# Kernel tuning notes

Hardware: AMD Instinct MI355X
Metric: run time of the kernel (lower is better)

## Reference

```python
import jax, jax.numpy as jnp
import numpy as np

N = 4096
M = 1024
APPERTURE = 250
L1, L2, L3, PRED = 1024, 512, 128, 1
EPS = 1e-6


def _layer_norm(x, gamma, beta):
    # torch x.std(-1) is unbiased (ddof=1)
    mean = jnp.mean(x, axis=-1, keepdims=True)
    std = jnp.std(x, axis=-1, ddof=1, keepdims=True)
    return gamma * (x - mean) / (std + EPS) + beta


def _self_attention(x, Wq, Wk, Wv, Wo, band_mask):
    # x: [n, m]; Linear(bias=False) => x @ W.T
    K = x @ Wk.T
    Q = (x @ Wq.T) * 0.06
    V = x @ Wv.T
    logits = Q @ K.T                      # [n, n]
    logits = jnp.where(band_mask, logits, -jnp.inf)  # keep |i-j| < apperture
    att = jax.nn.softmax(logits, axis=-1)
    # original: y = (V^T @ att)^T == att^T @ V  (note the transpose!)
    y = att.T @ V
    return y @ Wo.T, att


def setup_inputs() -> dict:
    key = jax.random.key(0)
    ks = jax.random.split(key, 20)
    s = 0.02
    inp = {
        'x1': jax.random.normal(ks[0], (1, N, M), jnp.float32),
        'x2': jax.random.normal(ks[1], (1, N, M), jnp.float32),
        'x3': jax.random.normal(ks[2], (1, N, M), jnp.float32),
        'Wq': jax.random.normal(ks[3], (M, M), jnp.float32) * s,
        'Wk': jax.random.normal(ks[4], (M, M), jnp.float32) * s,
        'Wv': jax.random.normal(ks[5], (M, M), jnp.float32) * s,
        'Wo': jax.random.normal(ks[6], (M, M), jnp.float32) * s,
        'ka_w': jax.random.normal(ks[7], (L1, M), jnp.float32) * s,
        'ka_b': jnp.zeros((L1,), jnp.float32),
        'kb_w': jax.random.normal(ks[8], (L2, L1), jnp.float32) * s,
        'kb_b': jnp.zeros((L2,), jnp.float32),
        'kc_w': jax.random.normal(ks[9], (L3, L2), jnp.float32) * s,
        'kc_b': jnp.zeros((L3,), jnp.float32),
        'kd_w': jax.random.normal(ks[10], (PRED, L3), jnp.float32) * s,
        'kd_b': jnp.zeros((PRED,), jnp.float32),
        'g13': jnp.ones((M,), jnp.float32),
        'b13': jnp.zeros((M,), jnp.float32),
        'gkc': jnp.ones((L3,), jnp.float32),
        'bkc': jnp.zeros((L3,), jnp.float32),
        'seq_len': N,
    }
    return inp


def reference(x1, x2, x3, Wq, Wk, Wv, Wo, ka_w, ka_b, kb_w, kb_b, kc_w, kc_b,
              kd_w, kd_b, g13, b13, gkc, bkc, seq_len):
    x1 = x1.reshape(-1, x1.shape[2])
    x2 = x2.reshape(-1, x2.shape[2])
    x3 = x3.reshape(-1, x3.shape[2])
    n = x1.shape[0]
    idx = jnp.arange(n)
    band_mask = jnp.abs(idx[:, None] - idx[None, :]) < APPERTURE  # allowed

    y1, att1 = _self_attention(x1, Wq, Wk, Wv, Wo, band_mask)
    y2, _ = _self_attention(x2, Wq, Wk, Wv, Wo, band_mask)
    y3, _ = _self_attention(x3, Wq, Wk, Wv, Wo, band_mask)

    # residual + (dropout == identity in eval) + shared LayerNorm
    y1 = _layer_norm(y1 + x1, g13, b13)
    y2 = _layer_norm(y2 + x2, g13, b13)
    y3 = _layer_norm(y3 + x3, g13, b13)

    y = y1 + y2 + y3  # cmb == [1,1,1]
    y = y @ ka_w.T + ka_b
    y = y @ kb_w.T + kb_b
    y = jax.nn.relu(y @ kc_w.T + kc_b)
    y = _layer_norm(y, gkc, bkc)
    y = jax.nn.sigmoid(y @ kd_w.T + kd_b)
    return y.reshape(1, -1), att1
```

## Files before the change

kernel.cpp:

```cpp
#include <hip/hip_runtime.h>
#include <hip/hip_bf16.h>
#include <cstdint>
#include <cstddef>

#define NSEQ 4096
#define MDIM 1024

typedef __attribute__((ext_vector_type(8))) short short8;
typedef __attribute__((ext_vector_type(4))) float f32x4;
typedef __attribute__((ext_vector_type(2))) long long2v;
typedef __attribute__((ext_vector_type(8))) int int8v;
typedef __attribute__((ext_vector_type(4))) int int4v;

typedef const __attribute__((address_space(1))) void gvoid_t;
typedef __attribute__((address_space(3))) void lvoid_t;

__device__ __forceinline__ unsigned short f2b(float x) {
  union { float f; unsigned int u; } a; a.f = x;
  unsigned int r = (a.u + 0x7fffu + ((a.u >> 16) & 1u)) >> 16;
  return (unsigned short)r;
}
__device__ __forceinline__ float b2f(unsigned short u) {
  union { float f; unsigned int u32; } a; a.u32 = ((unsigned int)u) << 16;
  return a.f;
}
__device__ __forceinline__ unsigned char f2e4(float x) {
  return (unsigned char)(__builtin_amdgcn_cvt_pk_fp8_f32(x, x, 0, false) & 0xff);
}
__device__ __forceinline__ unsigned int f2e4x4(float a, float b, float c, float d) {
  unsigned int lo = __builtin_amdgcn_cvt_pk_fp8_f32(a, b, 0, false);
  return (unsigned int)__builtin_amdgcn_cvt_pk_fp8_f32(c, d, lo, true);
}

__device__ __forceinline__ int8v pack32(const unsigned char* p0,
                                        const unsigned char* p1) {
  int4v lo = *(const int4v*)p0;
  int4v hi = *(const int4v*)p1;
  int8v r;
  r[0] = lo[0]; r[1] = lo[1]; r[2] = lo[2]; r[3] = lo[3];
  r[4] = hi[0]; r[5] = hi[1]; r[6] = hi[2]; r[7] = hi[3];
  return r;
}

__global__ __launch_bounds__(256) void k_cvt_all(
    const float* __restrict__ s0, const float* __restrict__ s1,
    const float* __restrict__ s2, const float* __restrict__ s3,
    const float* __restrict__ s4, const float* __restrict__ s5,
    const float* __restrict__ s6,
    const float* __restrict__ xa, const float* __restrict__ xb,
    const float* __restrict__ xc,
    unsigned char* __restrict__ Wf8, unsigned short* __restrict__ Wmlp,
    unsigned char* __restrict__ Xdst, float* __restrict__ sums) {
  int idx = blockIdx.x * 256 + threadIdx.x;
  if (idx < 1048576) {
    int seg = idx >> 18, local = idx & 262143;
    const float* src = (seg == 0) ? s0 : (seg == 1) ? s1 : (seg == 2) ? s2 : s3;
    float4 v = *(const float4*)(src + (size_t)local * 4);
    *(unsigned int*)(Wf8 + (size_t)idx * 4) =
        f2e4x4(v.x * 64.f, v.y * 64.f, v.z * 64.f, v.w * 64.f);
  } else if (idx < 1458176) {
    int i2 = idx - 1048576;
    const float* src; int local;
    if (i2 < 262144) { src = s4; local = i2; }
    else if (i2 < 393216) { src = s5; local = i2 - 262144; }
    else { src = s6; local = i2 - 393216; }
    float4 v = *(const float4*)(src + (size_t)local * 4);
    ushort4 o; o.x = f2b(v.x); o.y = f2b(v.y); o.z = f2b(v.z); o.w = f2b(v.w);
    *(ushort4*)(Wmlp + (size_t)i2 * 4) = o;
  } else if (idx < 4603904) {
    int i2 = idx - 1458176;
    int seg = i2 >> 20, local = i2 & 1048575;
    const float* src = (seg == 0) ? xa : (seg == 1) ? xb : xc;
    float4 v = *(const float4*)(src + (size_t)local * 4);
    *(unsigned int*)(Xdst + (size_t)i2 * 4) = f2e4x4(v.x, v.y, v.z, v.w);
  } else {
    int i3 = idx - 4603904;
    *(float4*)(sums + (size_t)i3 * 4) = make_float4(0.f, 0.f, 0.f, 0.f);
  }
}

template <int MODE, int OKIND, int DO_EXP, int DBUF>
__device__ __forceinline__ void gemm_core(
    const unsigned char* __restrict__ A, int lda,
    const unsigned char* __restrict__ B, int ldb,
    void* __restrict__ Cout, void* __restrict__ Cout2, int ldc,
    int K, float alpha,
    const unsigned char* __restrict__ A1, const unsigned char* __restrict__ A2,
    float* __restrict__ sums_out, unsigned char* __restrict__ smem) {
  int bx = blockIdx.x, by = blockIdx.y;
  const unsigned char* Ab;
  const unsigned char* Bb;
  void* Cdst = Cout;
  int k0 = 0, k1 = K, b_koff = 0;
  int ldce = ldc;
  int rbase, cbase;
  int ldae = lda, ldbe = ldb;
  if constexpr (MODE == 0) {
    Ab = A + (size_t)by * 128 * lda;
    Bb = B + (size_t)bx * 128 * ldb;
    rbase = bx * 128; cbase = by * 128;
  } else if constexpr (MODE == 3) {
    if (by < 16) {
      Ab = A + (size_t)by * 128 * lda;
      Bb = B + (size_t)bx * 128 * ldb;
      if (by >= 8) Cdst = Cout2;
      rbase = bx * 128; cbase = (by & 7) * 128;
    } else {
      Ab = B + (size_t)bx * 128 * ldb;
      Bb = A1 + (size_t)(by - 16) * 128 * 1024;
      Cdst = (void*)const_cast<unsigned char*>(A2);
      rbase = (by - 16) * 128; cbase = bx * 128;
      ldce = 3 * NSEQ;
    }
  } else if constexpr (MODE == 1) {
    int s = bx >> 5, ti = bx & 31;
    int bt = ti + by - 2;
    Ab = A + (size_t)(s * 32 + bt) * 128 * lda;
    Bb = B + (size_t)bx * 128 * ldb;
    rbase = bx * 128; cbase = by * 128;
  } else {
    int s = bx >> 5, ti = bx & 31;
    Ab = A + (size_t)by * 128 * lda + s * NSEQ;
    const unsigned char* Bbase = (s == 0) ? B : ((s == 1) ? A1 : A2);
    Bb = Bbase + (size_t)ti * 128 * 640;
    ldbe = 640;
    int lo = ti - 2; if (lo < 0) lo = 0;
    int hi = ti + 3; if (hi > 32) hi = 32;
    k0 = lo * 128; k1 = hi * 128;
    b_koff = (ti - 2) * 128;
    rbase = bx * 128; cbase = by * 128;
  }

  const int t = threadIdx.x;
  const int l = t & 63;
  const int w = t >> 6;
  const int fr = l & 15;
  const int quad = l >> 4;
  const int wm = (w >> 1) * 64;
  const int wn = (w & 1) * 64;
  const int fq4 = quad * 4;

  int srow[4], scg[4], sloff[4];
#pragma unroll
  for (int j = 0; j < 4; j++) {
    srow[j] = w * 32 + j * 8 + (l >> 3);
    scg[j] = ((l & 7) - srow[j]) & 7;
    sloff[j] = (w * 32 + j * 8) * 128 + l * 16;
  }

  f32x4 acc[4][4];
#pragma unroll
  for (int m = 0; m < 4; m++)
#pragma unroll
    for (int n = 0; n < 4; n++) acc[m][n] = (f32x4){0.f, 0.f, 0.f, 0.f};

  const int c0 = quad * 2;

  if constexpr (DBUF) {
    const int nt = (k1 - k0) >> 7;
    {
      int kk = k0, kb = kk - b_koff;
#pragma unroll
      for (int j = 0; j < 4; j++)
        __builtin_amdgcn_global_load_lds(
            (gvoid_t*)(Ab + (size_t)srow[j] * ldae + kk + scg[j] * 16),
            (lvoid_t*)(smem + sloff[j]), 16, 0, 0);
#pragma unroll
      for (int j = 0; j < 4; j++)
        __builtin_amdgcn_global_load_lds(
            (gvoid_t*)(Bb + (size_t)srow[j] * ldbe + kb + scg[j] * 16),
            (lvoid_t*)(smem + 16384 + sloff[j]), 16, 0, 0);
    }
    for (int tt = 0; tt < nt; tt++) {
      __syncthreads();
      if (tt + 1 < nt) {
        int kk = k0 + (tt + 1) * 128, kb = kk - b_koff;
        unsigned char* Asn = smem + ((tt + 1) & 1) * 32768;
#pragma unroll
        for (int j = 0; j < 4; j++)
          __builtin_amdgcn_global_load_lds(
              (gvoid_t*)(Ab + (size_t)srow[j] * ldae + kk + scg[j] * 16),
              (lvoid_t*)(Asn + sloff[j]), 16, 0, 0);
#pragma unroll
        for (int j = 0; j < 4; j++)
          __builtin_amdgcn_global_load_lds(
              (gvoid_t*)(Bb + (size_t)srow[j] * ldbe + kb + scg[j] * 16),
              (lvoid_t*)(Asn + 16384 + sloff[j]), 16, 0, 0);
      }
      const unsigned char* Asc = smem + (tt & 1) * 32768;
      const unsigned char* Bsc = Asc + 16384;
      int8v a8[4], b8[4];
#pragma unroll
      for (int m = 0; m < 4; m++) {
        int r = wm + m * 16 + fr;
        int s0i = (c0 + r) & 7, s1i = (s0i + 1) & 7;
        a8[m] = pack32(Asc + r * 128 + s0i * 16, Asc + r * 128 + s1i * 16);
      }
#pragma unroll
      for (int n = 0; n < 4; n++) {
        int r = wn + n * 16 + fr;
        int s0i = (c0 + r) & 7, s1i = (s0i + 1) & 7;
        b8[n] = pack32(Bsc + r * 128 + s0i * 16, Bsc + r * 128 + s1i * 16);
      }
#pragma unroll
      for (int m = 0; m < 4; m++)
#pragma unroll
        for (int n = 0; n < 4; n++)
          acc[m][n] = __builtin_amdgcn_mfma_scale_f32_16x16x128_f8f6f4(
              a8[m], b8[n], acc[m][n], 0, 0, 0, 0x7F7F7F7F, 0, 0x7F7F7F7F);
    }
  } else {
    unsigned char* As = smem;
    unsigned char* Bs = smem + 16384;
    for (int kk = k0; kk < k1; kk += 128) {
      int kb = kk - b_koff;
      __syncthreads();
#pragma unroll
      for (int j = 0; j < 4; j++)
        __builtin_amdgcn_global_load_lds(
            (gvoid_t*)(Ab + (size_t)srow[j] * ldae + kk + scg[j] * 16),
            (lvoid_t*)(As + sloff[j]), 16, 0, 0);
#pragma unroll
      for (int j = 0; j < 4; j++)
        __builtin_amdgcn_global_load_lds(
            (gvoid_t*)(Bb + (size_t)srow[j] * ldbe + kb + scg[j] * 16),
            (lvoid_t*)(Bs + sloff[j]), 16, 0, 0);
      __syncthreads();
      int8v a8[4], b8[4];
#pragma unroll
      for (int m = 0; m < 4; m++) {
        int r = wm + m * 16 + fr;
        int s0i = (c0 + r) & 7, s1i = (s0i + 1) & 7;
        a8[m] = pack32(As + r * 128 + s0i * 16, As + r * 128 + s1i * 16);
      }
#pragma unroll
      for (int n = 0; n < 4; n++) {
        int r = wn + n * 16 + fr;
        int s0i = (c0 + r) & 7, s1i = (s0i + 1) & 7;
        b8[n] = pack32(Bs + r * 128 + s0i * 16, Bs + r * 128 + s1i * 16);
      }
#pragma unroll
      for (int m = 0; m < 4; m++)
#pragma unroll
        for (int n = 0; n < 4; n++)
          acc[m][n] = __builtin_amdgcn_mfma_scale_f32_16x16x128_f8f6f4(
              a8[m], b8[n], acc[m][n], 0, 0, 0, 0x7F7F7F7F, 0, 0x7F7F7F7F);
    }
  }

  float rowsum[4] = {0.f, 0.f, 0.f, 0.f};
  const int jb = ((bx & 31) - 2) * 128;
#pragma unroll
  for (int m = 0; m < 4; m++) {
#pragma unroll
    for (int n = 0; n < 4; n++) {
      int oc = cbase + wm + m * 16 + fq4;
      int orow = rbase + wn + n * 16 + fr;
      float v0 = acc[m][n][0] * alpha, v1 = acc[m][n][1] * alpha;
      float v2 = acc[m][n][2] * alpha, v3 = acc[m][n][3] * alpha;
      if constexpr (OKIND == 1) {
        if constexpr (DO_EXP) {
          v0 = __expf(v0); v1 = __expf(v1); v2 = __expf(v2); v3 = __expf(v3);
          if constexpr (MODE == 1) {
            int d0 = (orow & 4095) - (jb + oc);
            rowsum[n] += ((unsigned)(d0 + 249) < 499u ? v0 : 0.f)
                       + ((unsigned)(d0 + 248) < 499u ? v1 : 0.f)
                       + ((unsigned)(d0 + 247) < 499u ? v2 : 0.f)
                       + ((unsigned)(d0 + 246) < 499u ? v3 : 0.f);
          }
        }
        ushort4 o; o.x = f2b(v0); o.y = f2b(v1); o.z = f2b(v2); o.w = f2b(v3);
        *(uint2*)((unsigned short*)Cdst + (size_t)orow * ldce + oc) = *(uint2*)&o;
      } else {
        *(unsigned int*)((unsigned char*)Cdst + (size_t)orow * ldce + oc) =
            f2e4x4(v0, v1, v2, v3);
      }
    }
  }
  if constexpr (MODE == 1 && DO_EXP) {
#pragma unroll
    for (int n = 0; n < 4; n++) {
      float sv = rowsum[n];
      sv += __shfl_xor(sv, 16);
      sv += __shfl_xor(sv, 32);
      if (quad == 0) {
        int orow = rbase + wn + n * 16 + fr;
        atomicAdd(sums_out + orow, sv);
      }
    }
  }
}

__global__ __launch_bounds__(256) void k_qkv(
    const unsigned char* __restrict__ A, const unsigned char* __restrict__ B,
    void* __restrict__ Cout, void* __restrict__ Cout2, float alpha,
    const unsigned char* __restrict__ A1, const unsigned char* __restrict__ A2) {
  __shared__ unsigned char smem[2 * 128 * 128];
  gemm_core<3, 2, 0, 0>(A, 1024, B, 1024, Cout, Cout2, 1024, 1024, alpha,
                        A1, A2, nullptr, smem);
}

__global__ __launch_bounds__(256) void k_logits(
    const unsigned char* __restrict__ A, const unsigned char* __restrict__ B,
    void* __restrict__ Cout, float alpha, float* __restrict__ sums) {
  int ti = blockIdx.x & 31;
  int bt = ti + (int)blockIdx.y - 2;
  if (bt < 0 || bt >= 32) return;
  __shared__ unsigned char smem[4 * 128 * 128];
  gemm_core<1, 1, 1, 1>(A, 1024, B, 1024, Cout, nullptr, 640, 1024, alpha,
                        nullptr, nullptr, sums, smem);
}

__global__ __launch_bounds__(256) void k_av(
    const unsigned char* __restrict__ A, const unsigned char* __restrict__ B,
    void* __restrict__ Cout, float alpha,
    const unsigned char* __restrict__ A1, const unsigned char* __restrict__ A2) {
  __shared__ unsigned char smem[4 * 128 * 128];
  gemm_core<2, 2, 0, 1>(A, 3 * NSEQ, B, 640, Cout, nullptr, 1024, NSEQ, alpha,
                        A1, A2, nullptr, smem);
}

__global__ __launch_bounds__(256) void k_wo(
    const unsigned char* __restrict__ A, const unsigned char* __restrict__ B,
    void* __restrict__ Cout, float alpha) {
  __shared__ unsigned char smem[4 * 128 * 128];
  gemm_core<0, 1, 0, 1>(A, 1024, B, 1024, Cout, nullptr, 1024, 1024, alpha,
                        nullptr, nullptr, nullptr, smem);
}

__global__ __launch_bounds__(256) void k_gemm64(
    const unsigned short* __restrict__ A, int lda,
    const unsigned short* __restrict__ B, int ldb,
    void* __restrict__ Cout, int ldc, int K,
    const float* __restrict__ bias, int relu, int out_bf16) {
  __shared__ unsigned short smem[4 * 64 * 64];
  int bx = blockIdx.x, by = blockIdx.y;
  const unsigned short* Ab = A + (size_t)by * 64 * lda;
  const unsigned short* Bb = B + (size_t)bx * 64 * ldb;
  int rbase = bx * 64, cbase = by * 64;

  const int t = threadIdx.x;
  const int l = t & 63;
  const int w = t >> 6;
  const int fr = l & 15;
  const int quad = l >> 4;
  const int wm = (w & 1) * 32;
  const int wn = (w >> 1) * 32;
  const int fq4 = quad * 4;

  int srow[2], scg[2], sloff[2];
#pragma unroll
  for (int j = 0; j < 2; j++) {
    srow[j] = w * 16 + j * 8 + (l >> 3);
    scg[j] = ((l & 7) - srow[j]) & 7;
    sloff[j] = (w * 16 + j * 8) * 64 + l * 8;
  }

  f32x4 acc[2][2];
#pragma unroll
  for (int m = 0; m < 2; m++)
#pragma unroll
    for (int n = 0; n < 2; n++) acc[m][n] = (f32x4){0.f, 0.f, 0.f, 0.f};

  const int nt = K >> 6;

#pragma unroll
  for (int j = 0; j < 2; j++)
    __builtin_amdgcn_global_load_lds(
        (gvoid_t*)(Ab + (size_t)srow[j] * lda + scg[j] * 8),
        (lvoid_t*)(smem + sloff[j]), 16, 0, 0);
#pragma unroll
  for (int j = 0; j < 2; j++)
    __builtin_amdgcn_global_load_lds(
        (gvoid_t*)(Bb + (size_t)srow[j] * ldb + scg[j] * 8),
        (lvoid_t*)(smem + 4096 + sloff[j]), 16, 0, 0);

  for (int tt = 0; tt < nt; tt++) {
    __syncthreads();
    if (tt + 1 < nt) {
      int kk = (tt + 1) * 64;
      unsigned short* Asn = smem + ((tt + 1) & 1) * 8192;
#pragma unroll
      for (int j = 0; j < 2; j++)
        __builtin_amdgcn_global_load_lds(
            (gvoid_t*)(Ab + (size_t)srow[j] * lda + kk + scg[j] * 8),
            (lvoid_t*)(Asn + sloff[j]), 16, 0, 0);
#pragma unroll
      for (int j = 0; j < 2; j++)
        __builtin_amdgcn_global_load_lds(
            (gvoid_t*)(Bb + (size_t)srow[j] * ldb + kk + scg[j] * 8),
            (lvoid_t*)(Asn + 4096 + sloff[j]), 16, 0, 0);
    }
    const unsigned short* Asc = smem + (tt & 1) * 8192;
    const unsigned short* Bsc = Asc + 4096;
#pragma unroll
    for (int s = 0; s < 2; s++) {
      short8 af[2], bf[2];
#pragma unroll
      for (int m = 0; m < 2; m++) {
        int r = wm + m * 16 + fr;
        int slot = (s * 4 + quad + r) & 7;
        af[m] = *(const short8*)(Asc + r * 64 + slot * 8);
      }
#pragma unroll
      for (int n = 0; n < 2; n++) {
        int r = wn + n * 16 + fr;
        int slot = (s * 4 + quad + r) & 7;
        bf[n] = *(const short8*)(Bsc + r * 64 + slot * 8);
      }
#pragma unroll
      for (int m = 0; m < 2; m++)
#pragma unroll
        for (int n = 0; n < 2; n++)
          acc[m][n] = __builtin_amdgcn_mfma_f32_16x16x32_bf16(af[m], bf[n], acc[m][n], 0, 0, 0);
    }
  }

#pragma unroll
  for (int m = 0; m < 2; m++) {
#pragma unroll
    for (int n = 0; n < 2; n++) {
      int oc = cbase + wm + m * 16 + fq4;
      int orow = rbase + wn + n * 16 + fr;
      float4 bv = bias ? *(const float4*)(bias + oc) : make_float4(0.f, 0.f, 0.f, 0.f);
      float v0 = acc[m][n][0] + bv.x, v1 = acc[m][n][1] + bv.y;
      float v2 = acc[m][n][2] + bv.z, v3 = acc[m][n][3] + bv.w;
      if (relu) {
        v0 = fmaxf(v0, 0.f); v1 = fmaxf(v1, 0.f);
        v2 = fmaxf(v2, 0.f); v3 = fmaxf(v3, 0.f);
      }
      if (out_bf16) {
        ushort4 o; o.x = f2b(v0); o.y = f2b(v1); o.z = f2b(v2); o.w = f2b(v3);
        *(uint2*)((unsigned short*)Cout + (size_t)orow * ldc + oc) = *(uint2*)&o;
      } else {
        *(float4*)((float*)Cout + (size_t)orow * ldc + oc) = make_float4(v0, v1, v2, v3);
      }
    }
  }
}

__global__ __launch_bounds__(256) void k_build_attT(const unsigned short* __restrict__ Eband,
                                                    const float* __restrict__ sums,
                                                    unsigned char* __restrict__ t0,
                                                    unsigned char* __restrict__ t1,
                                                    unsigned char* __restrict__ t2) {
  int byy = blockIdx.y;
  int s = byy >> 5, ti = byy & 31;
  int tj = ti + (int)blockIdx.x - 2;
  if (tj < 0 || tj >= 32) return;
  unsigned char* dst = (s == 0) ? t0 : ((s == 1) ? t1 : t2);
  __shared__ unsigned char T[128][132];
  int t = threadIdx.x;
  int c0 = (ti - tj + 2) * 128;
  int colg = (t & 31) * 4;
  for (int jj = t >> 5; jj < 128; jj += 8) {
    int jg = s * NSEQ + tj * 128 + jj;
    float inv = 16.f / sums[jg];
    ushort4 v = *(const ushort4*)&Eband[(size_t)jg * 640 + c0 + colg];
    float vv[4] = {b2f(v.x), b2f(v.y), b2f(v.z), b2f(v.w)};
#pragma unroll
    for (int q = 0; q < 4; q++) {
      int i = ti * 128 + colg + q;
      int d = i - (tj * 128 + jj);
      float a = (d < 250 && d > -250) ? vv[q] * inv : 0.f;
      T[colg + q][jj] = f2e4(a);
    }
  }
  __syncthreads();
  int jb0 = (tj - ti + 2) * 128;
  for (int ii = t >> 5; ii < 128; ii += 8) {
    size_t o = (size_t)(ti * 128 + ii) * 640 + jb0 + colg;
    *(unsigned int*)(dst + o) = *(const unsigned int*)&T[ii][colg];
  }
}

__global__ __launch_bounds__(256) void k_write_att(const unsigned short* __restrict__ Eband,
                                                   const float* __restrict__ sums,
                                                   float* __restrict__ att) {
  int i = blockIdx.x;
  int ti = i >> 7, cbase = (ti - 2) * 128;
  int jlo = i - 249; if (jlo < 0) jlo = 0;
  int jhi = i + 249; if (jhi > NSEQ - 1) jhi = NSEQ - 1;
  float inv = 1.f / sums[i];
  const unsigned short* L = Eband + (size_t)i * 640;
  float* arow = att + (size_t)i * NSEQ;
  for (int j0 = threadIdx.x * 4; j0 < NSEQ; j0 += 1024) {
    float ov[4];
#pragma unroll
    for (int q = 0; q < 4; q++) {
      int j = j0 + q;
      ov[q] = (j >= jlo && j <= jhi) ? b2f(L[j - cbase]) * inv : 0.f;
    }
    *(float4*)(arow + j0) = make_float4(ov[0], ov[1], ov[2], ov[3]);
  }
}

__global__ __launch_bounds__(256) void k_ln3(const unsigned short* __restrict__ yo,
                                             const float* __restrict__ x1,
                                             const float* __restrict__ x2,
                                             const float* __restrict__ x3,
                                             const float* __restrict__ g,
                                             const float* __restrict__ b,
                                             unsigned short* __restrict__ ysum_b) {
  int i = blockIdx.x, t = threadIdx.x;
  int w = t >> 6, lane = t & 63;
  __shared__ float red[8];
  const float* xs[3] = {x1, x2, x3};
  float4 gg = *(const float4*)(g + t * 4);
  float4 bb = *(const float4*)(b + t * 4);
  float acc[4] = {0.f, 0.f, 0.f, 0.f};
  for (int s = 0; s < 3; s++) {
    ushort4 yv = *(const ushort4*)(yo + ((size_t)(s * NSEQ + i)) * MDIM + t * 4);
    float4 xx = *(const float4*)(xs[s] + (size_t)i * MDIM + t * 4);
    float v[4] = {b2f(yv.x) + xx.x, b2f(yv.y) + xx.y, b2f(yv.z) + xx.z, b2f(yv.w) + xx.w};
    float s1 = v[0] + v[1] + v[2] + v[3];
    float s2 = v[0]*v[0] + v[1]*v[1] + v[2]*v[2] + v[3]*v[3];
    for (int off = 32; off; off >>= 1) { s1 += __shfl_xor(s1, off); s2 += __shfl_xor(s2, off); }
    __syncthreads();
    if (lane == 0) { red[w] = s1; red[4 + w] = s2; }
    __syncthreads();
    float S1 = red[0] + red[1] + red[2] + red[3];
    float S2 = red[4] + red[5] + red[6] + red[7];
    float mean = S1 * (1.f / 1024.f);
    float var = (S2 - S1 * mean) * (1.f / 1023.f);
    float rstd = 1.f / (sqrtf(var) + 1e-6f);
    acc[0] += gg.x * (v[0] - mean) * rstd + bb.x;
    acc[1] += gg.y * (v[1] - mean) * rstd + bb.y;
    acc[2] += gg.z * (v[2] - mean) * rstd + bb.z;
    acc[3] += gg.w * (v[3] - mean) * rstd + bb.w;
  }
  ushort4 o;
  o.x = f2b(acc[0]); o.y = f2b(acc[1]); o.z = f2b(acc[2]); o.w = f2b(acc[3]);
  *(ushort4*)(ysum_b + (size_t)i * MDIM + t * 4) = o;
}

__global__ __launch_bounds__(128) void k_final(const float* __restrict__ h3,
                                               const float* __restrict__ g,
                                               const float* __restrict__ b,
                                               const float* __restrict__ kdw,
                                               const float* __restrict__ kdb,
                                               float* __restrict__ yout) {
  int i = blockIdx.x, t = threadIdx.x;
  float v = h3[(size_t)i * 128 + t];
  float s1 = v, s2 = v * v;
  for (int off = 32; off; off >>= 1) { s1 += __shfl_xor(s1, off); s2 += __shfl_xor(s2, off); }
  __shared__ float red[4];
  int w = t >> 6, lane = t & 63;
  if (lane == 0) { red[w] = s1; red[2 + w] = s2; }
  __syncthreads();
  float S1 = red[0] + red[1], S2 = red[2] + red[3];
  float mean = S1 * (1.f / 128.f);
  float var = (S2 - S1 * mean) * (1.f / 127.f);
  float rstd = 1.f / (sqrtf(var) + 1e-6f);
  float ln = g[t] * (v - mean) * rstd + b[t];
  float p = ln * kdw[t];
  for (int off = 32; off; off >>= 1) p += __shfl_xor(p, off);
  __syncthreads();
  if (lane == 0) red[w] = p;
  __syncthreads();
  if (t == 0) {
    float z = red[0] + red[1] + kdb[0];
    yout[i] = 1.f / (1.f + __expf(-z));
  }
}

extern "C" void kernel_launch(void* const* d_in, const int* in_sizes, int n_in,
                              void* d_out, int out_size, void* d_ws, size_t ws_size,
                              hipStream_t stream) {
  const float* x1 = (const float*)d_in[0];
  const float* x2 = (const float*)d_in[1];
  const float* x3 = (const float*)d_in[2];
  const float* Wq = (const float*)d_in[3];
  const float* Wk = (const float*)d_in[4];
  const float* Wv = (const float*)d_in[5];
  const float* Wo = (const float*)d_in[6];
  const float* ka_w = (const float*)d_in[7];
  const float* ka_b = (const float*)d_in[8];
  const float* kb_w = (const float*)d_in[9];
  const float* kb_b = (const float*)d_in[10];
  const float* kc_w = (const float*)d_in[11];
  const float* kc_b = (const float*)d_in[12];
  const float* kd_w = (const float*)d_in[13];
  const float* kd_b = (const float*)d_in[14];
  const float* g13 = (const float*)d_in[15];
  const float* b13 = (const float*)d_in[16];
  const float* gkc = (const float*)d_in[17];
  const float* bkc = (const float*)d_in[18];

  float* y_out = (float*)d_out;
  float* att_out = y_out + NSEQ;

  char* ws = (char*)d_ws;
  size_t off = 0;
  auto alloc = [&](size_t bytes) -> void* {
    void* p = ws + off;
    off += (bytes + 255) & ~(size_t)255;
    return p;
  };
  const size_t NM = (size_t)3 * NSEQ * MDIM;
  unsigned char* Wf = (unsigned char*)alloc(4 * 1048576);
  unsigned short* Wmlp = (unsigned short*)alloc((1048576 + 524288 + 65536) * 2);
  unsigned char* Xf = (unsigned char*)alloc(NM);
  unsigned char* Qf = (unsigned char*)alloc(NM);
  unsigned char* Kf = (unsigned char*)alloc(NM);
  unsigned char* VTf = (unsigned char*)alloc(NM);
  unsigned short* Eband = (unsigned short*)alloc((size_t)3 * NSEQ * 640 * 2);
  float* sums = (float*)alloc((size_t)3 * NSEQ * 4);
  unsigned char* aT0 = (unsigned char*)alloc((size_t)NSEQ * 640);
  unsigned char* aT1 = (unsigned char*)alloc((size_t)NSEQ * 640);
  unsigned char* aT2 = (unsigned char*)alloc((size_t)NSEQ * 640);
  unsigned char* Wv_f = Wf + 2097152;
  unsigned char* Wo_f = Wf + 3145728;
  unsigned short* ka_b16 = Wmlp;
  unsigned short* kb_b16 = Wmlp + 1048576;
  unsigned short* kc_b16 = Wmlp + 1572864;
  unsigned char* yb = Xf;
  unsigned short* yo = (unsigned short*)Qf;
  unsigned short* ysum_b = (unsigned short*)VTf;
  unsigned short* h1b = (unsigned short*)Xf;
  unsigned short* h2b = (unsigned short*)Qf;
  float* h3 = (float*)aT0;

  k_cvt_all<<<17996, 256, 0, stream>>>(Wq, Wk, Wv, Wo, ka_w, kb_w, kc_w,
                                       x1, x2, x3, Wf, Wmlp, Xf, sums);

  k_qkv<<<dim3(96, 24), 256, 0, stream>>>(Wf, Xf, Qf, Kf, 1.f / 64.f, Wv_f, VTf);
  k_logits<<<dim3(96, 5), 256, 0, stream>>>(Kf, Qf, Eband, 0.06f, sums);
  k_build_attT<<<dim3(5, 96), 256, 0, stream>>>(Eband, sums, aT0, aT1, aT2);
  k_av<<<dim3(96, 8), 256, 0, stream>>>(VTf, aT0, yb, 0.5f, aT1, aT2);
  k_write_att<<<4096, 256, 0, stream>>>(Eband, sums, att_out);
  k_wo<<<dim3(96, 8), 256, 0, stream>>>(Wo_f, yb, yo, 1.f / 512.f);
  k_ln3<<<4096, 256, 0, stream>>>(yo, x1, x2, x3, g13, b13, ysum_b);

  k_gemm64<<<dim3(64, 16), 256, 0, stream>>>(ka_b16, 1024, ysum_b, 1024, h1b, 1024,
                                             1024, ka_b, 0, 1);
  k_gemm64<<<dim3(64, 8), 256, 0, stream>>>(kb_b16, 1024, h1b, 1024, h2b, 512,
                                            1024, kb_b, 0, 1);
  k_gemm64<<<dim3(64, 2), 256, 0, stream>>>(kc_b16, 512, h2b, 512, h3, 128,
                                            512, kc_b, 1, 0);
  k_final<<<4096, 128, 0, stream>>>(h3, gkc, bkc, kd_w, kd_b, y_out);
}
```

Before: 335.2 us.

## Use 256-wide K tiles for dense GEMMs, fine-grained waits in AV, merge att kernels

The qkv, logits and wo GEMMs now load 256-deep K tiles into a single buffer, with a 16-way swizzle, replacing the 128-deep tiles and the double buffering some of them used. This halves the number of barrier rounds per tile. The banded AV GEMM gets its own double-buffered core that uses explicit vmcnt waits and raw s_barrier so the prefetch overlaps compute. The attention-transpose build and the full att write are merged into one launch to drop a kernel boundary. In exchange, logits and wo lose their double-buffer overlap, and the larger tiles raise LDS use.

```diff
diff --git a/kernel.cpp b/kernel.cpp
--- a/kernel.cpp
+++ b/kernel.cpp
@@ -79,8 +79,8 @@
   }
 }
 
-template <int MODE, int OKIND, int DO_EXP, int DBUF>
-__device__ __forceinline__ void gemm_core(
+template <int MODE, int OKIND, int DO_EXP>
+__device__ __forceinline__ void gemm_core256(
     const unsigned char* __restrict__ A, int lda,
     const unsigned char* __restrict__ B, int ldb,
     void* __restrict__ Cout, void* __restrict__ Cout2, int ldc,
@@ -91,7 +91,6 @@
   const unsigned char* Ab;
   const unsigned char* Bb;
   void* Cdst = Cout;
-  int k0 = 0, k1 = K, b_koff = 0;
   int ldce = ldc;
   int rbase, cbase;
   int ldae = lda, ldbe = ldb;
@@ -112,22 +111,11 @@
       rbase = (by - 16) * 128; cbase = bx * 128;
       ldce = 3 * NSEQ;
     }
-  } else if constexpr (MODE == 1) {
+  } else {
     int s = bx >> 5, ti = bx & 31;
     int bt = ti + by - 2;
     Ab = A + (size_t)(s * 32 + bt) * 128 * lda;
     Bb = B + (size_t)bx * 128 * ldb;
-    rbase = bx * 128; cbase = by * 128;
-  } else {
-    int s = bx >> 5, ti = bx & 31;
-    Ab = A + (size_t)by * 128 * lda + s * NSEQ;
-    const unsigned char* Bbase = (s == 0) ? B : ((s == 1) ? A1 : A2);
-    Bb = Bbase + (size_t)ti * 128 * 640;
-    ldbe = 640;
-    int lo = ti - 2; if (lo < 0) lo = 0;
-    int hi = ti + 3; if (hi > 32) hi = 32;
-    k0 = lo * 128; k1 = hi * 128;
-    b_koff = (ti - 2) * 128;
     rbase = bx * 128; cbase = by * 128;
   }
 
@@ -140,13 +128,16 @@
   const int wn = (w & 1) * 64;
   const int fq4 = quad * 4;
 
-  int srow[4], scg[4], sloff[4];
-#pragma unroll
-  for (int j = 0; j < 4; j++) {
-    srow[j] = w * 32 + j * 8 + (l >> 3);
-    scg[j] = ((l & 7) - srow[j]) & 7;
-    sloff[j] = (w * 32 + j * 8) * 128 + l * 16;
-  }
+  int srow[8], scg[8], sloff[8];
+#pragma unroll
+  for (int j = 0; j < 8; j++) {
+    srow[j] = w * 32 + j * 4 + (l >> 4);
+    scg[j] = ((l & 15) - srow[j]) & 15;
+    sloff[j] = (w * 32 + j * 4) * 256 + l * 16;
+  }
+
+  unsigned char* As = smem;
+  unsigned char* Bs = smem + 32768;
 
   f32x4 acc[4][4];
 #pragma unroll
@@ -154,90 +145,36 @@
 #pragma unroll
     for (int n = 0; n < 4; n++) acc[m][n] = (f32x4){0.f, 0.f, 0.f, 0.f};
 
-  const int c0 = quad * 2;
-
-  if constexpr (DBUF) {
-    const int nt = (k1 - k0) >> 7;
-    {
-      int kk = k0, kb = kk - b_koff;
-#pragma unroll
-      for (int j = 0; j < 4; j++)
-        __builtin_amdgcn_global_load_lds(
-            (gvoid_t*)(Ab + (size_t)srow[j] * ldae + kk + scg[j] * 16),
-            (lvoid_t*)(smem + sloff[j]), 16, 0, 0);
-#pragma unroll
-      for (int j = 0; j < 4; j++)
-        __builtin_amdgcn_global_load_lds(
-            (gvoid_t*)(Bb + (size_t)srow[j] * ldbe + kb + scg[j] * 16),
-            (lvoid_t*)(smem + 16384 + sloff[j]), 16, 0, 0);
-    }
-    for (int tt = 0; tt < nt; tt++) {
-      __syncthreads();
-      if (tt + 1 < nt) {
-        int kk = k0 + (tt + 1) * 128, kb = kk - b_koff;
-        unsigned char* Asn = smem + ((tt + 1) & 1) * 32768;
-#pragma unroll
-        for (int j = 0; j < 4; j++)
-          __builtin_amdgcn_global_load_lds(
-              (gvoid_t*)(Ab + (size_t)srow[j] * ldae + kk + scg[j] * 16),
-              (lvoid_t*)(Asn + sloff[j]), 16, 0, 0);
-#pragma unroll
-        for (int j = 0; j < 4; j++)
-          __builtin_amdgcn_global_load_lds(
-              (gvoid_t*)(Bb + (size_t)srow[j] * ldbe + kb + scg[j] * 16),
-              (lvoid_t*)(Asn + 16384 + sloff[j]), 16, 0, 0);
-      }
-      const unsigned char* Asc = smem + (tt & 1) * 32768;
-      const unsigned char* Bsc = Asc + 16384;
+  const int nt = K >> 8;
+  for (int tt = 0; tt < nt; tt++) {
+    int kk = tt * 256;
+    __syncthreads();
+#pragma unroll
+    for (int j = 0; j < 8; j++)
+      __builtin_amdgcn_global_load_lds(
+          (gvoid_t*)(Ab + (size_t)srow[j] * ldae + kk + scg[j] * 16),
+          (lvoid_t*)(As + sloff[j]), 16, 0, 0);
+#pragma unroll
+    for (int j = 0; j < 8; j++)
+      __builtin_amdgcn_global_load_lds(
+          (gvoid_t*)(Bb + (size_t)srow[j] * ldbe + kk + scg[j] * 16),
+          (lvoid_t*)(Bs + sloff[j]), 16, 0, 0);
+    __syncthreads();
+#pragma unroll
+    for (int h = 0; h < 2; h++) {
+      const int cb = h * 8 + quad * 2;
       int8v a8[4], b8[4];
 #pragma unroll
       for (int m = 0; m < 4; m++) {
         int r = wm + m * 16 + fr;
-        int s0i = (c0 + r) & 7, s1i = (s0i + 1) & 7;
-        a8[m] = pack32(Asc + r * 128 + s0i * 16, Asc + r * 128 + s1i * 16);
+        int s0i = (cb + r) & 15, s1i = (cb + 1 + r) & 15;
+        a8[m] = pack32(As + r * 256 + s0i * 16, As + r * 256 + s1i * 16);
       }
 #pragma unroll
       for (int n = 0; n < 4; n++) {
         int r = wn + n * 16 + fr;
-        int s0i = (c0 + r) & 7, s1i = (s0i + 1) & 7;
-        b8[n] = pack32(Bsc + r * 128 + s0i * 16, Bsc + r * 128 + s1i * 16);
-      }
-#pragma unroll
-      for (int m = 0; m < 4; m++)
-#pragma unroll
-        for (int n = 0; n < 4; n++)
-          acc[m][n] = __builtin_amdgcn_mfma_scale_f32_16x16x128_f8f6f4(
-              a8[m], b8[n], acc[m][n], 0, 0, 0, 0x7F7F7F7F, 0, 0x7F7F7F7F);
-    }
-  } else {
-    unsigned char* As = smem;
-    unsigned char* Bs = smem + 16384;
-    for (int kk = k0; kk < k1; kk += 128) {
-      int kb = kk - b_koff;
-      __syncthreads();
-#pragma unroll
-      for (int j = 0; j < 4; j++)
-        __builtin_amdgcn_global_load_lds(
-            (gvoid_t*)(Ab + (size_t)srow[j] * ldae + kk + scg[j] * 16),
-            (lvoid_t*)(As + sloff[j]), 16, 0, 0);
-#pragma unroll
-      for (int j = 0; j < 4; j++)
-        __builtin_amdgcn_global_load_lds(
-            (gvoid_t*)(Bb + (size_t)srow[j] * ldbe + kb + scg[j] * 16),
-            (lvoid_t*)(Bs + sloff[j]), 16, 0, 0);
-      __syncthreads();
-      int8v a8[4], b8[4];
-#pragma unroll
-      for (int m = 0; m < 4; m++) {
-        int r = wm + m * 16 + fr;
-        int s0i = (c0 + r) & 7, s1i = (s0i + 1) & 7;
-        a8[m] = pack32(As + r * 128 + s0i * 16, As + r * 128 + s1i * 16);
-      }
-#pragma unroll
-      for (int n = 0; n < 4; n++) {
-        int r = wn + n * 16 + fr;
-        int s0i = (c0 + r) & 7, s1i = (s0i + 1) & 7;
-        b8[n] = pack32(Bs + r * 128 + s0i * 16, Bs + r * 128 + s1i * 16);
+        int s0i = (cb + r) & 15, s1i = (cb + 1 + r) & 15;
+        b8[n] = pack32(Bs + r * 256 + s0i * 16, Bs + r * 256 + s1i * 16);
       }
 #pragma unroll
       for (int m = 0; m < 4; m++)
@@ -291,12 +228,129 @@
   }
 }
 
+__device__ __forceinline__ void gemm_core_av(
+    const unsigned char* __restrict__ A, int lda,
+    const unsigned char* __restrict__ B,
+    void* __restrict__ Cout, int ldc, float alpha,
+    const unsigned char* __restrict__ A1, const unsigned char* __restrict__ A2,
+    unsigned char* __restrict__ smem) {
+  int bx = blockIdx.x, by = blockIdx.y;
+  int s = bx >> 5, ti = bx & 31;
+  const unsigned char* Ab = A + (size_t)by * 128 * lda + s * NSEQ;
+  const unsigned char* Bbase = (s == 0) ? B : ((s == 1) ? A1 : A2);
+  const unsigned char* Bb = Bbase + (size_t)ti * 128 * 640;
+  const int ldbe = 640;
+  int lo = ti - 2; if (lo < 0) lo = 0;
+  int hi = ti + 3; if (hi > 32) hi = 32;
+  int k0 = lo * 128, k1 = hi * 128;
+  int b_koff = (ti - 2) * 128;
+  int rbase = bx * 128, cbase = by * 128;
+
+  const int t = threadIdx.x;
+  const int l = t & 63;
+  const int w = t >> 6;
+  const int fr = l & 15;
+  const int quad = l >> 4;
+  const int wm = (w >> 1) * 64;
+  const int wn = (w & 1) * 64;
+  const int fq4 = quad * 4;
+
+  int srow[4], scg[4], sloff[4];
+#pragma unroll
+  for (int j = 0; j < 4; j++) {
+    srow[j] = w * 32 + j * 8 + (l >> 3);
+    scg[j] = ((l & 7) - srow[j]) & 7;
+    sloff[j] = (w * 32 + j * 8) * 128 + l * 16;
+  }
+
+  f32x4 acc[4][4];
+#pragma unroll
+  for (int m = 0; m < 4; m++)
+#pragma unroll
+    for (int n = 0; n < 4; n++) acc[m][n] = (f32x4){0.f, 0.f, 0.f, 0.f};
+
+  const int c0 = quad * 2;
+  const int nt = (k1 - k0) >> 7;
+
+  {
+    int kk = k0, kb = kk - b_koff;
+#pragma unroll
+    for (int j = 0; j < 4; j++)
+      __builtin_amdgcn_global_load_lds(
+          (gvoid_t*)(Ab + (size_t)srow[j] * lda + kk + scg[j] * 16),
+          (lvoid_t*)(smem + sloff[j]), 16, 0, 0);
+#pragma unroll
+    for (int j = 0; j < 4; j++)
+      __builtin_amdgcn_global_load_lds(
+          (gvoid_t*)(Bb + (size_t)srow[j] * ldbe + kb + scg[j] * 16),
+          (lvoid_t*)(smem + 16384 + sloff[j]), 16, 0, 0);
+  }
+
+  for (int tt = 0; tt < nt; tt++) {
+    if (tt + 1 < nt) {
+      int kk = k0 + (tt + 1) * 128, kb = kk - b_koff;
+      unsigned char* Asn = smem + ((tt + 1) & 1) * 32768;
+#pragma unroll
+      for (int j = 0; j < 4; j++)
+        __builtin_amdgcn_global_load_lds(
+            (gvoid_t*)(Ab + (size_t)srow[j] * lda + kk + scg[j] * 16),
+            (lvoid_t*)(Asn + sloff[j]), 16, 0, 0);
+#pragma unroll
+      for (int j = 0; j < 4; j++)
+        __builtin_amdgcn_global_load_lds(
+            (gvoid_t*)(Bb + (size_t)srow[j] * ldbe + kb + scg[j] * 16),
+            (lvoid_t*)(Asn + 16384 + sloff[j]), 16, 0, 0);
+      __builtin_amdgcn_sched_barrier(0);
+      asm volatile("s_waitcnt vmcnt(8)" ::: "memory");
+    } else {
+      asm volatile("s_waitcnt vmcnt(0)" ::: "memory");
+    }
+    asm volatile("s_barrier" ::: "memory");
+
+    const unsigned char* Asc = smem + (tt & 1) * 32768;
+    const unsigned char* Bsc = Asc + 16384;
+    int8v a8[4], b8[4];
+#pragma unroll
+    for (int m = 0; m < 4; m++) {
+      int r = wm + m * 16 + fr;
+      int s0i = (c0 + r) & 7, s1i = (s0i + 1) & 7;
+      a8[m] = pack32(Asc + r * 128 + s0i * 16, Asc + r * 128 + s1i * 16);
+    }
+#pragma unroll
+    for (int n = 0; n < 4; n++) {
+      int r = wn + n * 16 + fr;
+      int s0i = (c0 + r) & 7, s1i = (s0i + 1) & 7;
+      b8[n] = pack32(Bsc + r * 128 + s0i * 16, Bsc + r * 128 + s1i * 16);
+    }
+#pragma unroll
+    for (int m = 0; m < 4; m++)
+#pragma unroll
+      for (int n = 0; n < 4; n++)
+        acc[m][n] = __builtin_amdgcn_mfma_scale_f32_16x16x128_f8f6f4(
+            a8[m], b8[n], acc[m][n], 0, 0, 0, 0x7F7F7F7F, 0, 0x7F7F7F7F);
+    asm volatile("s_barrier" ::: "memory");
+  }
+
+#pragma unroll
+  for (int m = 0; m < 4; m++) {
+#pragma unroll
+    for (int n = 0; n < 4; n++) {
+      int oc = cbase + wm + m * 16 + fq4;
+      int orow = rbase + wn + n * 16 + fr;
+      float v0 = acc[m][n][0] * alpha, v1 = acc[m][n][1] * alpha;
+      float v2 = acc[m][n][2] * alpha, v3 = acc[m][n][3] * alpha;
+      *(unsigned int*)((unsigned char*)Cout + (size_t)orow * ldc + oc) =
+          f2e4x4(v0, v1, v2, v3);
+    }
+  }
+}
+
 __global__ __launch_bounds__(256) void k_qkv(
     const unsigned char* __restrict__ A, const unsigned char* __restrict__ B,
     void* __restrict__ Cout, void* __restrict__ Cout2, float alpha,
     const unsigned char* __restrict__ A1, const unsigned char* __restrict__ A2) {
-  __shared__ unsigned char smem[2 * 128 * 128];
-  gemm_core<3, 2, 0, 0>(A, 1024, B, 1024, Cout, Cout2, 1024, 1024, alpha,
+  __shared__ unsigned char smem[2 * 128 * 256];
+  gemm_core256<3, 2, 0>(A, 1024, B, 1024, Cout, Cout2, 1024, 1024, alpha,
                         A1, A2, nullptr, smem);
 }
 
@@ -306,8 +360,8 @@
   int ti = blockIdx.x & 31;
   int bt = ti + (int)blockIdx.y - 2;
   if (bt < 0 || bt >= 32) return;
-  __shared__ unsigned char smem[4 * 128 * 128];
-  gemm_core<1, 1, 1, 1>(A, 1024, B, 1024, Cout, nullptr, 640, 1024, alpha,
+  __shared__ unsigned char smem[2 * 128 * 256];
+  gemm_core256<1, 1, 1>(A, 1024, B, 1024, Cout, nullptr, 640, 1024, alpha,
                         nullptr, nullptr, sums, smem);
 }
 
@@ -316,15 +370,14 @@
     void* __restrict__ Cout, float alpha,
     const unsigned char* __restrict__ A1, const unsigned char* __restrict__ A2) {
   __shared__ unsigned char smem[4 * 128 * 128];
-  gemm_core<2, 2, 0, 1>(A, 3 * NSEQ, B, 640, Cout, nullptr, 1024, NSEQ, alpha,
-                        A1, A2, nullptr, smem);
+  gemm_core_av(A, 3 * NSEQ, B, Cout, 1024, alpha, A1, A2, smem);
 }
 
 __global__ __launch_bounds__(256) void k_wo(
     const unsigned char* __restrict__ A, const unsigned char* __restrict__ B,
     void* __restrict__ Cout, float alpha) {
-  __shared__ unsigned char smem[4 * 128 * 128];
-  gemm_core<0, 1, 0, 1>(A, 1024, B, 1024, Cout, nullptr, 1024, 1024, alpha,
+  __shared__ unsigned char smem[2 * 128 * 256];
+  gemm_core256<0, 1, 0>(A, 1024, B, 1024, Cout, nullptr, 1024, 1024, alpha,
                         nullptr, nullptr, nullptr, smem);
 }
 
@@ -439,59 +492,60 @@
   }
 }
 
-__global__ __launch_bounds__(256) void k_build_attT(const unsigned short* __restrict__ Eband,
-                                                    const float* __restrict__ sums,
-                                                    unsigned char* __restrict__ t0,
-                                                    unsigned char* __restrict__ t1,
-                                                    unsigned char* __restrict__ t2) {
-  int byy = blockIdx.y;
-  int s = byy >> 5, ti = byy & 31;
-  int tj = ti + (int)blockIdx.x - 2;
-  if (tj < 0 || tj >= 32) return;
-  unsigned char* dst = (s == 0) ? t0 : ((s == 1) ? t1 : t2);
+__global__ __launch_bounds__(256) void k_attw(const unsigned short* __restrict__ Eband,
+                                              const float* __restrict__ sums,
+                                              unsigned char* __restrict__ t0,
+                                              unsigned char* __restrict__ t1,
+                                              unsigned char* __restrict__ t2,
+                                              float* __restrict__ att) {
   __shared__ unsigned char T[128][132];
-  int t = threadIdx.x;
-  int c0 = (ti - tj + 2) * 128;
-  int colg = (t & 31) * 4;
-  for (int jj = t >> 5; jj < 128; jj += 8) {
-    int jg = s * NSEQ + tj * 128 + jj;
-    float inv = 16.f / sums[jg];
-    ushort4 v = *(const ushort4*)&Eband[(size_t)jg * 640 + c0 + colg];
-    float vv[4] = {b2f(v.x), b2f(v.y), b2f(v.z), b2f(v.w)};
-#pragma unroll
-    for (int q = 0; q < 4; q++) {
-      int i = ti * 128 + colg + q;
-      int d = i - (tj * 128 + jj);
-      float a = (d < 250 && d > -250) ? vv[q] * inv : 0.f;
-      T[colg + q][jj] = f2e4(a);
-    }
-  }
-  __syncthreads();
-  int jb0 = (tj - ti + 2) * 128;
-  for (int ii = t >> 5; ii < 128; ii += 8) {
-    size_t o = (size_t)(ti * 128 + ii) * 640 + jb0 + colg;
-    *(unsigned int*)(dst + o) = *(const unsigned int*)&T[ii][colg];
-  }
-}
-
-__global__ __launch_bounds__(256) void k_write_att(const unsigned short* __restrict__ Eband,
-                                                   const float* __restrict__ sums,
-                                                   float* __restrict__ att) {
-  int i = blockIdx.x;
-  int ti = i >> 7, cbase = (ti - 2) * 128;
-  int jlo = i - 249; if (jlo < 0) jlo = 0;
-  int jhi = i + 249; if (jhi > NSEQ - 1) jhi = NSEQ - 1;
-  float inv = 1.f / sums[i];
-  const unsigned short* L = Eband + (size_t)i * 640;
-  float* arow = att + (size_t)i * NSEQ;
-  for (int j0 = threadIdx.x * 4; j0 < NSEQ; j0 += 1024) {
-    float ov[4];
-#pragma unroll
-    for (int q = 0; q < 4; q++) {
-      int j = j0 + q;
-      ov[q] = (j >= jlo && j <= jhi) ? b2f(L[j - cbase]) * inv : 0.f;
-    }
-    *(float4*)(arow + j0) = make_float4(ov[0], ov[1], ov[2], ov[3]);
+  int bid = blockIdx.x;
+  if (bid < 480) {
+    int tjoff = bid % 5;
+    int byy = bid / 5;
+    int s = byy >> 5, ti = byy & 31;
+    int tj = ti + tjoff - 2;
+    if (tj < 0 || tj >= 32) return;
+    unsigned char* dst = (s == 0) ? t0 : ((s == 1) ? t1 : t2);
+    int t = threadIdx.x;
+    int c0 = (ti - tj + 2) * 128;
+    int colg = (t & 31) * 4;
+    for (int jj = t >> 5; jj < 128; jj += 8) {
+      int jg = s * NSEQ + tj * 128 + jj;
+      float inv = 16.f / sums[jg];
+      ushort4 v = *(const ushort4*)&Eband[(size_t)jg * 640 + c0 + colg];
+      float vv[4] = {b2f(v.x), b2f(v.y), b2f(v.z), b2f(v.w)};
+#pragma unroll
+      for (int q = 0; q < 4; q++) {
+        int i = ti * 128 + colg + q;
+        int d = i - (tj * 128 + jj);
+        float a = (d < 250 && d > -250) ? vv[q] * inv : 0.f;
+        T[colg + q][jj] = f2e4(a);
+      }
+    }
+    __syncthreads();
+    int jb0 = (tj - ti + 2) * 128;
+    for (int ii = t >> 5; ii < 128; ii += 8) {
+      size_t o = (size_t)(ti * 128 + ii) * 640 + jb0 + colg;
+      *(unsigned int*)(dst + o) = *(const unsigned int*)&T[ii][colg];
+    }
+  } else {
+    int i = bid - 480;
+    int ti = i >> 7, cbase = (ti - 2) * 128;
+    int jlo = i - 249; if (jlo < 0) jlo = 0;
+    int jhi = i + 249; if (jhi > NSEQ - 1) jhi = NSEQ - 1;
+    float inv = 1.f / sums[i];
+    const unsigned short* L = Eband + (size_t)i * 640;
+    float* arow = att + (size_t)i * NSEQ;
+    for (int j0 = threadIdx.x * 4; j0 < NSEQ; j0 += 1024) {
+      float ov[4];
+#pragma unroll
+      for (int q = 0; q < 4; q++) {
+        int j = j0 + q;
+        ov[q] = (j >= jlo && j <= jhi) ? b2f(L[j - cbase]) * inv : 0.f;
+      }
+      *(float4*)(arow + j0) = make_float4(ov[0], ov[1], ov[2], ov[3]);
+    }
   }
 }
 
@@ -626,9 +680,8 @@
 
   k_qkv<<<dim3(96, 24), 256, 0, stream>>>(Wf, Xf, Qf, Kf, 1.f / 64.f, Wv_f, VTf);
   k_logits<<<dim3(96, 5), 256, 0, stream>>>(Kf, Qf, Eband, 0.06f, sums);
-  k_build_attT<<<dim3(5, 96), 256, 0, stream>>>(Eband, sums, aT0, aT1, aT2);
+  k_attw<<<4576, 256, 0, stream>>>(Eband, sums, aT0, aT1, aT2, att_out);
   k_av<<<dim3(96, 8), 256, 0, stream>>>(VTf, aT0, yb, 0.5f, aT1, aT2);
-  k_write_att<<<4096, 256, 0, stream>>>(Eband, sums, att_out);
   k_wo<<<dim3(96, 8), 256, 0, stream>>>(Wo_f, yb, yo, 1.f / 512.f);
   k_ln3<<<4096, 256, 0, stream>>>(yo, x1, x2, x3, g13, b13, ysum_b);
 
```

New measurement: 322.9 us. 1.04x faster.
